# Kernel tuning notes

Hardware: AMD Instinct MI355X
Metric: run time of the kernel (lower is better)

The kernel has to match this reference:

```python
import jax, jax.numpy as jnp
import numpy as np

N = 50000   # nodes
E = 800000  # edges (before self-loops)
B = 256     # graphs in batch
F = 128     # input feature dim
H = 4       # heads per layer
C = 64      # out_channels per head
NEG_SLOPE = 0.2


def setup_inputs() -> dict:
    key = jax.random.key(0)
    ks = jax.random.split(key, 16)
    s = 0.05
    inp = {
        "x": jax.random.normal(ks[0], (N, F), dtype=jnp.float32),
        "edge_index": jax.random.randint(ks[1], (2, E), 0, N, dtype=jnp.int32),
        "batch": jnp.sort(jax.random.randint(ks[2], (N,), 0, B, dtype=jnp.int32)),
        # layer 1: F -> H*C
        "W1": jax.random.normal(ks[3], (F, H * C), dtype=jnp.float32) * s,
        "as1": jax.random.normal(ks[4], (H, C), dtype=jnp.float32) * s,
        "ad1": jax.random.normal(ks[5], (H, C), dtype=jnp.float32) * s,
        "b1": jnp.zeros((H * C,), dtype=jnp.float32),
        # layer 2: H*C -> H*C
        "W2": jax.random.normal(ks[6], (H * C, H * C), dtype=jnp.float32) * s,
        "as2": jax.random.normal(ks[7], (H, C), dtype=jnp.float32) * s,
        "ad2": jax.random.normal(ks[8], (H, C), dtype=jnp.float32) * s,
        "b2": jnp.zeros((H * C,), dtype=jnp.float32),
        # layer 3: H*C -> H*C
        "W3": jax.random.normal(ks[9], (H * C, H * C), dtype=jnp.float32) * s,
        "as3": jax.random.normal(ks[10], (H, C), dtype=jnp.float32) * s,
        "ad3": jax.random.normal(ks[11], (H, C), dtype=jnp.float32) * s,
        "b3": jnp.zeros((H * C,), dtype=jnp.float32),
    }
    return inp


def _gat_layer(x, src, dst, W, a_src, a_dst, bias):
    """PyG GATConv (concat=True, self-loops already included in src/dst)."""
    n = x.shape[0]
    xh = (x @ W).reshape(n, H, C)                      # [N,H,C]
    alpha_s = jnp.sum(xh * a_src, axis=-1)             # [N,H]
    alpha_d = jnp.sum(xh * a_dst, axis=-1)             # [N,H]
    logits = alpha_s[src] + alpha_d[dst]               # [E',H]
    logits = jnp.where(logits > 0, logits, NEG_SLOPE * logits)  # LeakyReLU
    # segment-wise softmax over destination neighborhoods
    m = jax.lax.stop_gradient(jax.ops.segment_max(logits, dst, num_segments=n))
    e = jnp.exp(logits - m[dst])
    z = jax.ops.segment_sum(e, dst, num_segments=n)
    alpha = e / (z[dst] + 1e-16)                       # [E',H]
    msg = xh[src] * alpha[:, :, None]                  # [E',H,C]
    out = jax.ops.segment_sum(msg, dst, num_segments=n)  # [N,H,C]
    return out.reshape(n, H * C) + bias


def reference(x, edge_index, batch, W1, as1, ad1, b1, W2, as2, ad2, b2, W3, as3, ad3, b3):
    n = x.shape[0]
    loops = jnp.arange(n, dtype=edge_index.dtype)
    src = jnp.concatenate([edge_index[0], loops])
    dst = jnp.concatenate([edge_index[1], loops])
    # dropout is identity at inference; activation = ReLU between layers
    h = jax.nn.relu(_gat_layer(x, src, dst, W1, as1, ad1, b1))
    h = jax.nn.relu(_gat_layer(h, src, dst, W2, as2, ad2, b2))
    h = _gat_layer(h, src, dst, W3, as3, ad3, b3)
    pooled = jax.ops.segment_max(h, batch, num_segments=B)  # global max pool -> [B, H*C]
    return jnp.squeeze(pooled)
```

## Files before the change

kernel.cpp:

```cpp
#include <hip/hip_runtime.h>
#include <hip/hip_fp16.h>
#include <math.h>

#define NN 50000
#define NE 800000
#define NT 850000
#define NB 256
#define FIN 128
#define HC 256
#define NH 4
#define CD 64
#define NEG 0.2f
#define SCAN_B 196
#define PSPL 8

typedef _Float16 half8 __attribute__((ext_vector_type(8)));
typedef _Float16 half4v __attribute__((ext_vector_type(4)));
typedef float f32x4 __attribute__((ext_vector_type(4)));

__device__ __forceinline__ void gld16(const void* g, void* l) {
    __builtin_amdgcn_global_load_lds(
        (const __attribute__((address_space(1))) void*)g,
        (__attribute__((address_space(3))) void*)l, 16, 0, 0);
}


__global__ void zero_int_kernel(int* __restrict__ p, int n) {
    int i = blockIdx.x * blockDim.x + threadIdx.x;
    if (i < n) p[i] = 0;
}

__global__ void hist_kernel(const int* __restrict__ ei, int* __restrict__ cnt) {
    int e = blockIdx.x * blockDim.x + threadIdx.x;
    if (e < NE) {
        atomicAdd(&cnt[ei[NE + e]], 1);
    } else if (e < NT) {
        atomicAdd(&cnt[e - NE], 1);
    }
}

__global__ __launch_bounds__(256) void part_kernel(const int* __restrict__ cnt,
                                                   int* __restrict__ part) {
    __shared__ int red[4];
    int i = blockIdx.x * 256 + threadIdx.x;
    int v = (i < NN) ? cnt[i] : 0;
#pragma unroll
    for (int off = 32; off > 0; off >>= 1) v += __shfl_down(v, off);
    if ((threadIdx.x & 63) == 0) red[threadIdx.x >> 6] = v;
    __syncthreads();
    if (threadIdx.x == 0) part[blockIdx.x] = red[0] + red[1] + red[2] + red[3];
}

__global__ __launch_bounds__(256) void offs_kernel(const int* __restrict__ part,
                                                   int* __restrict__ boff) {
    __shared__ int sh[256];
    int t = threadIdx.x;
    sh[t] = (t < SCAN_B) ? part[t] : 0;
    __syncthreads();
    for (int off = 1; off < 256; off <<= 1) {
        int add = (t >= off) ? sh[t - off] : 0;
        __syncthreads();
        sh[t] += add;
        __syncthreads();
    }
    boff[t] = (t == 0) ? 0 : sh[t - 1];
}

__global__ __launch_bounds__(256) void write_scan_kernel(const int* __restrict__ cnt,
        const int* __restrict__ boff, int* __restrict__ rowptr, int* __restrict__ cursor) {
    __shared__ int sh[256];
    int t = threadIdx.x;
    int i = blockIdx.x * 256 + t;
    int v = (i < NN) ? cnt[i] : 0;
    sh[t] = v;
    __syncthreads();
    for (int off = 1; off < 256; off <<= 1) {
        int add = (t >= off) ? sh[t - off] : 0;
        __syncthreads();
        sh[t] += add;
        __syncthreads();
    }
    int run = boff[blockIdx.x] + sh[t] - v;
    if (i < NN) { rowptr[i] = run; cursor[i] = run; }
    if (i == NN - 1) rowptr[NN] = run + v;
}

__global__ void scatter_kernel(const int* __restrict__ ei, int* __restrict__ cursor,
                               int* __restrict__ colsrc) {
    int e = blockIdx.x * blockDim.x + threadIdx.x;
    int s, d;
    if (e < NE)      { s = ei[e]; d = ei[NE + e]; }
    else if (e < NT) { s = e - NE; d = s; }
    else return;
    int pos = atomicAdd(&cursor[d], 1);
    colsrc[pos] = s;
}

__global__ void batch_bounds_kernel(const int* __restrict__ batch, int* __restrict__ bstart) {
    int i = blockIdx.x * blockDim.x + threadIdx.x;
    if (i >= NN) return;
    int b = batch[i];
    if (i == 0) {
        for (int bb = 0; bb <= b; ++bb) bstart[bb] = 0;
    } else {
        int pb = batch[i - 1];
        if (pb != b) for (int bb = pb + 1; bb <= b; ++bb) bstart[bb] = i;
    }
    if (i == NN - 1) {
        for (int bb = b + 1; bb <= NB; ++bb) bstart[bb] = NN;
    }
}


__global__ __launch_bounds__(256) void split_x_kernel(const float* __restrict__ X,
        _Float16* __restrict__ Xh, _Float16* __restrict__ Xl) {
    int i = blockIdx.x * 256 + threadIdx.x;
    if (i >= NN * FIN / 4) return;
    float4 v = reinterpret_cast<const float4*>(X)[i];
    half4v h, l;
    h[0] = (_Float16)v.x; h[1] = (_Float16)v.y; h[2] = (_Float16)v.z; h[3] = (_Float16)v.w;
    l[0] = (_Float16)(v.x - (float)h[0]);
    l[1] = (_Float16)(v.y - (float)h[1]);
    l[2] = (_Float16)(v.z - (float)h[2]);
    l[3] = (_Float16)(v.w - (float)h[3]);
    reinterpret_cast<half4v*>(Xh)[i] = h;
    reinterpret_cast<half4v*>(Xl)[i] = l;
}


template<int K>
__global__ __launch_bounds__(256) void wprep_kernel(const float* __restrict__ W,
                                                    _Float16* __restrict__ WtS) {
    __shared__ float sm[8][257];
    const int t = threadIdx.x;
    const int b = blockIdx.x;
    const int kb = b * 8;
    const bool lo3 = (kb >= 2 * K);
    const int kphys = lo3 ? kb - 2 * K : (kb >= K ? kb - K : kb);
#pragma unroll
    for (int i = 0; i < 8; ++i) {
        int idx = i * 256 + t;
        sm[idx >> 8][idx & 255] = W[(size_t)(kphys + (idx >> 8)) * HC + (idx & 255)];
    }
    __syncthreads();
    half8 o;
#pragma unroll
    for (int r = 0; r < 8; ++r) {
        float w = sm[r][t];
        _Float16 h = (_Float16)w;
        o[r] = lo3 ? (_Float16)(w - (float)h) : h;
    }
    *reinterpret_cast<half8*>(&WtS[((size_t)b * 256 + t) * 8]) = o;
}


template<int K>
__global__ __launch_bounds__(256) void mfma_gemm_kernel(
        const _Float16* __restrict__ Xh, const _Float16* __restrict__ Xl,
        const _Float16* __restrict__ WtS, __half* __restrict__ XHo,
        const float* __restrict__ as_g, const float* __restrict__ ad_g,
        float* __restrict__ aS, float* __restrict__ aD) {
    constexpr int C3 = 3 * K;
    constexpr int NSTEP = C3 / 32;
    constexpr int SPP = K / 32;
    __shared__ __align__(16) _Float16 As[4][64 * 32];
    __shared__ __align__(16) _Float16 Bs[4][32 * 256];
    const int t = threadIdx.x;
    const int lane = t & 63;
    const int wid = t >> 6;
    const int wm = wid & 1, wn = wid >> 1;
    const int r0 = blockIdx.x * 64;
    const int l15 = lane & 15;
    const int kcl = lane >> 4;
    const int kcA = t >> 6;
    const int arow = min(r0 + ((t & 63) ^ kcA), NN - 1);

    f32x4 acc[2][8];
#pragma unroll
    for (int i = 0; i < 2; ++i)
#pragma unroll
        for (int j = 0; j < 8; ++j) acc[i][j] = (f32x4)0.f;

    auto issue = [&](int s) {
        const int sel = s / SPP;
        const int cbase = (s - sel * SPP) * 32;
        const _Float16* srcA = (sel == 1) ? Xl : Xh;
        const int buf = s & 3;
        gld16(srcA + (size_t)arow * K + cbase + kcA * 8, &As[buf][t * 8]);
        const _Float16* bsrc = WtS + (size_t)s * (32 * 256);
#pragma unroll
        for (int r = 0; r < 4; ++r)
            gld16(bsrc + ((size_t)r * 256 + t) * 8, &Bs[buf][(r * 256 + t) * 8]);
    };
    auto mfma_step = [&](int s) {
        const int buf = s & 3;
        half8 a0 = *reinterpret_cast<const half8*>(
            &As[buf][(kcl * 64 + ((wm * 32      + l15) ^ kcl)) * 8]);
        half8 a1 = *reinterpret_cast<const half8*>(
            &As[buf][(kcl * 64 + ((wm * 32 + 16 + l15) ^ kcl)) * 8]);
        const _Float16* bp = &Bs[buf][(kcl * 256 + wn * 128 + l15) * 8];
        __builtin_amdgcn_s_setprio(1);
#pragma unroll
        for (int nf = 0; nf < 8; ++nf) {
            half8 b = *reinterpret_cast<const half8*>(bp + nf * 16 * 8);
            acc[0][nf] = __builtin_amdgcn_mfma_f32_16x16x32_f16(a0, b, acc[0][nf], 0, 0, 0);
            acc[1][nf] = __builtin_amdgcn_mfma_f32_16x16x32_f16(a1, b, acc[1][nf], 0, 0, 0);
        }
        __builtin_amdgcn_s_setprio(0);
    };

    issue(0); issue(1); issue(2);
    asm volatile("s_waitcnt vmcnt(10)" ::: "memory");
    __builtin_amdgcn_s_barrier();
    __builtin_amdgcn_sched_barrier(0);

    for (int s = 0; s < NSTEP - 3; ++s) {
        issue(s + 3);
        mfma_step(s);
        asm volatile("s_waitcnt vmcnt(10) lgkmcnt(0)" ::: "memory");
        __builtin_amdgcn_s_barrier();
        __builtin_amdgcn_sched_barrier(0);
    }
    mfma_step(NSTEP - 3);
    asm volatile("s_waitcnt vmcnt(5) lgkmcnt(0)" ::: "memory");
    __builtin_amdgcn_s_barrier();
    __builtin_amdgcn_sched_barrier(0);
    mfma_step(NSTEP - 2);
    asm volatile("s_waitcnt vmcnt(0) lgkmcnt(0)" ::: "memory");
    __builtin_amdgcn_s_barrier();
    __builtin_amdgcn_sched_barrier(0);
    mfma_step(NSTEP - 1);

    const int rb = r0 + wm * 32 + (lane >> 4) * 4;
    const int cb = wn * 128 + l15;
    float asv[8], adv[8];
#pragma unroll
    for (int nf = 0; nf < 8; ++nf) {
        asv[nf] = as_g[cb + nf * 16];
        adv[nf] = ad_g[cb + nf * 16];
    }
#pragma unroll
    for (int mf = 0; mf < 2; ++mf)
#pragma unroll
        for (int r = 0; r < 4; ++r) {
            int row = rb + mf * 16 + r;
            float s0 = 0.f, s1 = 0.f, d0 = 0.f, d1 = 0.f;
#pragma unroll
            for (int nf = 0; nf < 4; ++nf) {
                float a = acc[mf][nf][r], b = acc[mf][nf + 4][r];
                s0 += a * asv[nf];     d0 += a * adv[nf];
                s1 += b * asv[nf + 4]; d1 += b * adv[nf + 4];
            }
#pragma unroll
            for (int off = 1; off < 16; off <<= 1) {
                s0 += __shfl_xor(s0, off); s1 += __shfl_xor(s1, off);
                d0 += __shfl_xor(d0, off); d1 += __shfl_xor(d1, off);
            }
            if (row < NN) {
                if (l15 == 0) {
                    aS[row * 4 + 2 * wn] = s0; aS[row * 4 + 2 * wn + 1] = s1;
                    aD[row * 4 + 2 * wn] = d0; aD[row * 4 + 2 * wn + 1] = d1;
                }
#pragma unroll
                for (int nf = 0; nf < 8; ++nf)
                    XHo[(size_t)row * HC + cb + nf * 16] = __float2half(acc[mf][nf][r]);
            }
        }
}


#define LEAKY(v) ((v) > 0.f ? (v) : NEG * (v))

template<int RELU, int SPLIT>
__global__ __launch_bounds__(256) void aggregate_kernel(
        const int* __restrict__ rowptr, const int* __restrict__ colsrc,
        const float* __restrict__ aS, const float* __restrict__ aD,
        const __half* __restrict__ XH,
        const float* __restrict__ bias, float* __restrict__ OUT,
        __half* __restrict__ OUTh, __half* __restrict__ OUTl) {
    __shared__ float4 wbuf[4][64];
    __shared__ int    ibuf[4][64];
    const int wslot = threadIdx.x >> 6;
    int n = blockIdx.x * 4 + wslot;
    int lane = threadIdx.x & 63;
    bool lo = lane < 32;
    const __half2* xbase = reinterpret_cast<const __half2*>(XH);
    float4 adv = *reinterpret_cast<const float4*>(aD + n * 4);
    float zl = 0.f, zh = 0.f;
    float al0 = 0.f, al1 = 0.f, ah0 = 0.f, ah1 = 0.f;
    int jb = rowptr[n], je = rowptr[n + 1];
    for (int c0 = jb; c0 < je; c0 += 64) {
        int cnt = min(64, je - c0);
        {
            int e = min(c0 + lane, je - 1);
            int s = colsrc[e];
            float4 sv = *reinterpret_cast<const float4*>(aS + s * 4);
            float4 w;
            w.x = __expf(LEAKY(sv.x + adv.x));
            w.y = __expf(LEAKY(sv.y + adv.y));
            w.z = __expf(LEAKY(sv.z + adv.z));
            w.w = __expf(LEAKY(sv.w + adv.w));
            wbuf[wslot][lane] = w;
            ibuf[wslot][lane] = s;
        }
        int u = 0;
        for (; u + 8 <= cnt; u += 8) {
            int sidx[8];
            float4 w[8];
#pragma unroll
            for (int k = 0; k < 8; ++k) { sidx[k] = ibuf[wslot][u + k]; w[k] = wbuf[wslot][u + k]; }
            __half2 p[8], q[8];
#pragma unroll
            for (int k = 0; k < 8; ++k) {
                const __half2* xp = xbase + (size_t)sidx[k] * (HC / 2) + lane;
                p[k] = xp[0];
                q[k] = xp[64];
            }
#pragma unroll
            for (int k = 0; k < 8; ++k) {
                float wl = lo ? w[k].x : w[k].y, wh = lo ? w[k].z : w[k].w;
                float2 f = __half22float2(p[k]);
                al0 += wl * f.x; al1 += wl * f.y;
                f = __half22float2(q[k]);
                ah0 += wh * f.x; ah1 += wh * f.y;
                zl += wl; zh += wh;
            }
        }
        for (; u < cnt; ++u) {
            int s0 = ibuf[wslot][u];
            float4 w0 = wbuf[wslot][u];
            const __half2* xp = xbase + (size_t)s0 * (HC / 2) + lane;
            __half2 p0 = xp[0], q0 = xp[64];
            float w0l = lo ? w0.x : w0.y, w0h = lo ? w0.z : w0.w;
            float2 f = __half22float2(p0);
            al0 += w0l * f.x; al1 += w0l * f.y;
            f = __half22float2(q0);
            ah0 += w0h * f.x; ah1 += w0h * f.y;
            zl += w0l; zh += w0h;
        }
    }
    float izl = 1.f / (zl + 1e-16f), izh = 1.f / (zh + 1e-16f);
    float2 bl = reinterpret_cast<const float2*>(bias)[lane];
    float2 bh = reinterpret_cast<const float2*>(bias + 128)[lane];
    float o0 = al0 * izl + bl.x;
    float o1 = al1 * izl + bl.y;
    float o2 = ah0 * izh + bh.x;
    float o3 = ah1 * izh + bh.y;
    if (RELU) {
        o0 = fmaxf(o0, 0.f); o1 = fmaxf(o1, 0.f);
        o2 = fmaxf(o2, 0.f); o3 = fmaxf(o3, 0.f);
    }
    if (SPLIT) {
        __half h0 = __float2half(o0), h1 = __float2half(o1);
        __half h2 = __float2half(o2), h3 = __float2half(o3);
        __half2* ph = reinterpret_cast<__half2*>(OUTh + (size_t)n * HC) + lane;
        ph[0]  = __half2(h0, h1);
        ph[64] = __half2(h2, h3);
        __half2* pl = reinterpret_cast<__half2*>(OUTl + (size_t)n * HC) + lane;
        pl[0]  = __half2(__float2half(o0 - __half2float(h0)), __float2half(o1 - __half2float(h1)));
        pl[64] = __half2(__float2half(o2 - __half2float(h2)), __float2half(o3 - __half2float(h3)));
    } else {
        float2* op = reinterpret_cast<float2*>(OUT + (size_t)n * HC) + lane;
        op[0]  = make_float2(o0, o1);
        op[64] = make_float2(o2, o3);
    }
}


__global__ __launch_bounds__(256) void pool1_kernel(const float* __restrict__ Hf,
        const int* __restrict__ bstart, float* __restrict__ part) {
    int b = blockIdx.x / PSPL, sp = blockIdx.x % PSPL;
    int c = threadIdx.x;
    int i0 = bstart[b], i1 = bstart[b + 1];
    float m = -INFINITY;
    for (int i = i0 + sp; i < i1; i += PSPL) m = fmaxf(m, Hf[(size_t)i * HC + c]);
    part[(size_t)blockIdx.x * HC + c] = m;
}

__global__ __launch_bounds__(256) void pool2_kernel(const float* __restrict__ part,
        float* __restrict__ out) {
    int b = blockIdx.x;
    int c = threadIdx.x;
    float m = -INFINITY;
#pragma unroll
    for (int sp = 0; sp < PSPL; ++sp)
        m = fmaxf(m, part[(size_t)(b * PSPL + sp) * HC + c]);
    out[b * HC + c] = m;
}


extern "C" void kernel_launch(void* const* d_in, const int* in_sizes, int n_in,
                              void* d_out, int out_size, void* d_ws, size_t ws_size,
                              hipStream_t stream) {
    const float* x     = (const float*)d_in[0];
    const int*   ei    = (const int*)d_in[1];
    const int*   batch = (const int*)d_in[2];
    const float* W1  = (const float*)d_in[3];
    const float* as1 = (const float*)d_in[4];
    const float* ad1 = (const float*)d_in[5];
    const float* b1  = (const float*)d_in[6];
    const float* W2  = (const float*)d_in[7];
    const float* as2 = (const float*)d_in[8];
    const float* ad2 = (const float*)d_in[9];
    const float* b2  = (const float*)d_in[10];
    const float* W3  = (const float*)d_in[11];
    const float* as3 = (const float*)d_in[12];
    const float* ad3 = (const float*)d_in[13];
    const float* b3  = (const float*)d_in[14];
    float* out = (float*)d_out;

    __half* Hh  = (__half*)d_ws;
    __half* Hl  = Hh + (size_t)NN * HC;
    __half* XHh = Hl + (size_t)NN * HC;
    _Float16* Xh1 = (_Float16*)Hh;
    _Float16* Xl1 = Xh1 + (size_t)NN * FIN;
    float* bufB = (float*)Hh;
    _Float16* WtS = (_Float16*)(XHh + (size_t)NN * HC);
    float*  aS  = (float*)(WtS + 768 * 256);
    float*  aD  = aS + NN * NH;
    float*  ppart = aD + NN * NH;
    int* cnt    = (int*)(ppart + (size_t)NB * PSPL * HC);
    int* rowptr = cnt + NN;
    int* cursor = rowptr + (NN + 1);
    int* colsrc = cursor + NN;
    int* bstart = colsrc + NT;
    int* part   = bstart + (NB + 1);
    int* boff   = part + SCAN_B;

    zero_int_kernel<<<(NN + 255) / 256, 256, 0, stream>>>(cnt, NN);
    hist_kernel<<<(NT + 255) / 256, 256, 0, stream>>>(ei, cnt);
    part_kernel<<<SCAN_B, 256, 0, stream>>>(cnt, part);
    offs_kernel<<<1, 256, 0, stream>>>(part, boff);
    write_scan_kernel<<<SCAN_B, 256, 0, stream>>>(cnt, boff, rowptr, cursor);
    scatter_kernel<<<(NT + 255) / 256, 256, 0, stream>>>(ei, cursor, colsrc);
    batch_bounds_kernel<<<(NN + 255) / 256, 256, 0, stream>>>(batch, bstart);

    const int gemm_grid = (NN + 63) / 64;
    const int node_grid = NN / 4;

    split_x_kernel<<<(NN * FIN / 4 + 255) / 256, 256, 0, stream>>>(x, Xh1, Xl1);

    wprep_kernel<FIN><<<3 * FIN / 8, 256, 0, stream>>>(W1, WtS);
    mfma_gemm_kernel<FIN><<<gemm_grid, 256, 0, stream>>>(
        Xh1, Xl1, WtS, XHh, as1, ad1, aS, aD);
    aggregate_kernel<1, 1><<<node_grid, 256, 0, stream>>>(rowptr, colsrc, aS, aD, XHh, b1,
                                                          nullptr, Hh, Hl);

    wprep_kernel<HC><<<3 * HC / 8, 256, 0, stream>>>(W2, WtS);
    mfma_gemm_kernel<HC><<<gemm_grid, 256, 0, stream>>>(
        (_Float16*)Hh, (_Float16*)Hl, WtS, XHh, as2, ad2, aS, aD);
    aggregate_kernel<1, 1><<<node_grid, 256, 0, stream>>>(rowptr, colsrc, aS, aD, XHh, b2,
                                                          nullptr, Hh, Hl);

    wprep_kernel<HC><<<3 * HC / 8, 256, 0, stream>>>(W3, WtS);
    mfma_gemm_kernel<HC><<<gemm_grid, 256, 0, stream>>>(
        (_Float16*)Hh, (_Float16*)Hl, WtS, XHh, as3, ad3, aS, aD);
    aggregate_kernel<0, 0><<<node_grid, 256, 0, stream>>>(rowptr, colsrc, aS, aD, XHh, b3,
                                                          bufB, nullptr, nullptr);

    pool1_kernel<<<NB * PSPL, 256, 0, stream>>>(bufB, bstart, ppart);
    pool2_kernel<<<NB, 256, 0, stream>>>(ppart, out);
}
```

Measured before the change: 468.1 us.

## Fuse fp32 hi/lo split into GEMM A-load and restage pipeline through registers

Removes the separate split_x kernel and instead converts fp32 input to hi/lo fp16 inside the layer-1 GEMM while staging A through registers. The GEMM pipeline drops from four to three LDS buffers, and A tiles are written to LDS by threads rather than by direct global-to-LDS loads. This avoids a full round-trip of the split input through memory, at the cost of register pressure and a different latency-hiding structure. Each aggregation is also launched as two half-sized grids, which adds launch overhead.

```diff
diff --git a/kernel.cpp b/kernel.cpp
--- a/kernel.cpp
+++ b/kernel.cpp
@@ -15,7 +15,6 @@
 #define PSPL 8
 
 typedef _Float16 half8 __attribute__((ext_vector_type(8)));
-typedef _Float16 half4v __attribute__((ext_vector_type(4)));
 typedef float f32x4 __attribute__((ext_vector_type(4)));
 
 __device__ __forceinline__ void gld16(const void* g, void* l) {
@@ -112,22 +111,6 @@
 }
 
 
-__global__ __launch_bounds__(256) void split_x_kernel(const float* __restrict__ X,
-        _Float16* __restrict__ Xh, _Float16* __restrict__ Xl) {
-    int i = blockIdx.x * 256 + threadIdx.x;
-    if (i >= NN * FIN / 4) return;
-    float4 v = reinterpret_cast<const float4*>(X)[i];
-    half4v h, l;
-    h[0] = (_Float16)v.x; h[1] = (_Float16)v.y; h[2] = (_Float16)v.z; h[3] = (_Float16)v.w;
-    l[0] = (_Float16)(v.x - (float)h[0]);
-    l[1] = (_Float16)(v.y - (float)h[1]);
-    l[2] = (_Float16)(v.z - (float)h[2]);
-    l[3] = (_Float16)(v.w - (float)h[3]);
-    reinterpret_cast<half4v*>(Xh)[i] = h;
-    reinterpret_cast<half4v*>(Xl)[i] = l;
-}
-
-
 template<int K>
 __global__ __launch_bounds__(256) void wprep_kernel(const float* __restrict__ W,
                                                     _Float16* __restrict__ WtS) {
@@ -154,17 +137,18 @@
 }
 
 
-template<int K>
+template<int K, bool F32IN>
 __global__ __launch_bounds__(256) void mfma_gemm_kernel(
         const _Float16* __restrict__ Xh, const _Float16* __restrict__ Xl,
+        const float* __restrict__ Xf,
         const _Float16* __restrict__ WtS, __half* __restrict__ XHo,
         const float* __restrict__ as_g, const float* __restrict__ ad_g,
         float* __restrict__ aS, float* __restrict__ aD) {
     constexpr int C3 = 3 * K;
     constexpr int NSTEP = C3 / 32;
     constexpr int SPP = K / 32;
-    __shared__ __align__(16) _Float16 As[4][64 * 32];
-    __shared__ __align__(16) _Float16 Bs[4][32 * 256];
+    __shared__ __align__(16) _Float16 As[3][64 * 32];
+    __shared__ __align__(16) _Float16 Bs[3][32 * 256];
     const int t = threadIdx.x;
     const int lane = t & 63;
     const int wid = t >> 6;
@@ -172,8 +156,9 @@
     const int r0 = blockIdx.x * 64;
     const int l15 = lane & 15;
     const int kcl = lane >> 4;
-    const int kcA = t >> 6;
-    const int arow = min(r0 + ((t & 63) ^ kcA), NN - 1);
+    const int srowA = t >> 2;
+    const int skcA  = t & 3;
+    const int arow = min(r0 + srowA, NN - 1);
 
     f32x4 acc[2][8];
 #pragma unroll
@@ -181,19 +166,43 @@
 #pragma unroll
         for (int j = 0; j < 8; ++j) acc[i][j] = (f32x4)0.f;
 
-    auto issue = [&](int s) {
+    auto loadA = [&](int s, float4& v0, float4& v1) {
         const int sel = s / SPP;
         const int cbase = (s - sel * SPP) * 32;
-        const _Float16* srcA = (sel == 1) ? Xl : Xh;
-        const int buf = s & 3;
-        gld16(srcA + (size_t)arow * K + cbase + kcA * 8, &As[buf][t * 8]);
+        if constexpr (F32IN) {
+            const float* p = Xf + (size_t)arow * K + cbase + skcA * 8;
+            v0 = *reinterpret_cast<const float4*>(p);
+            v1 = *reinterpret_cast<const float4*>(p + 4);
+        } else {
+            const _Float16* src = (sel == 1) ? Xl : Xh;
+            v0 = *reinterpret_cast<const float4*>(src + (size_t)arow * K + cbase + skcA * 8);
+        }
+    };
+    auto writeA = [&](int s, int buf, float4 v0, float4 v1) {
+        _Float16* d = &As[buf][(skcA * 64 + (srowA ^ skcA)) * 8];
+        if constexpr (F32IN) {
+            const int sel = s / SPP;
+            float f[8];
+            *reinterpret_cast<float4*>(f) = v0;
+            *reinterpret_cast<float4*>(f + 4) = v1;
+            half8 h;
+#pragma unroll
+            for (int e = 0; e < 8; ++e) {
+                _Float16 a = (_Float16)f[e];
+                h[e] = (sel == 1) ? (_Float16)(f[e] - (float)a) : a;
+            }
+            *reinterpret_cast<half8*>(d) = h;
+        } else {
+            *reinterpret_cast<float4*>(d) = v0;
+        }
+    };
+    auto issueB = [&](int s, int buf) {
         const _Float16* bsrc = WtS + (size_t)s * (32 * 256);
 #pragma unroll
         for (int r = 0; r < 4; ++r)
             gld16(bsrc + ((size_t)r * 256 + t) * 8, &Bs[buf][(r * 256 + t) * 8]);
     };
-    auto mfma_step = [&](int s) {
-        const int buf = s & 3;
+    auto mfma_step = [&](int s, int buf) {
         half8 a0 = *reinterpret_cast<const half8*>(
             &As[buf][(kcl * 64 + ((wm * 32      + l15) ^ kcl)) * 8]);
         half8 a1 = *reinterpret_cast<const half8*>(
@@ -209,27 +218,34 @@
         __builtin_amdgcn_s_setprio(0);
     };
 
-    issue(0); issue(1); issue(2);
-    asm volatile("s_waitcnt vmcnt(10)" ::: "memory");
+    float4 a00, a01, aN1_0, aN1_1, aN2_0, aN2_1;
+    loadA(0, a00, a01);
+    issueB(0, 0);
+    loadA(1, aN1_0, aN1_1);
+    issueB(1, 1);
+    writeA(0, 0, a00, a01);
+    if constexpr (F32IN) asm volatile("s_waitcnt vmcnt(6) lgkmcnt(0)" ::: "memory");
+    else                 asm volatile("s_waitcnt vmcnt(5) lgkmcnt(0)" ::: "memory");
     __builtin_amdgcn_s_barrier();
     __builtin_amdgcn_sched_barrier(0);
 
-    for (int s = 0; s < NSTEP - 3; ++s) {
-        issue(s + 3);
-        mfma_step(s);
-        asm volatile("s_waitcnt vmcnt(10) lgkmcnt(0)" ::: "memory");
+    for (int s = 0; s < NSTEP - 2; ++s) {
+        loadA(s + 2, aN2_0, aN2_1);
+        issueB(s + 2, (s + 2) % 3);
+        mfma_step(s, s % 3);
+        writeA(s + 1, (s + 1) % 3, aN1_0, aN1_1);
+        if constexpr (F32IN) asm volatile("s_waitcnt vmcnt(6) lgkmcnt(0)" ::: "memory");
+        else                 asm volatile("s_waitcnt vmcnt(5) lgkmcnt(0)" ::: "memory");
         __builtin_amdgcn_s_barrier();
         __builtin_amdgcn_sched_barrier(0);
-    }
-    mfma_step(NSTEP - 3);
-    asm volatile("s_waitcnt vmcnt(5) lgkmcnt(0)" ::: "memory");
-    __builtin_amdgcn_s_barrier();
-    __builtin_amdgcn_sched_barrier(0);
-    mfma_step(NSTEP - 2);
+        aN1_0 = aN2_0; aN1_1 = aN2_1;
+    }
+    mfma_step(NSTEP - 2, (NSTEP - 2) % 3);
+    writeA(NSTEP - 1, (NSTEP - 1) % 3, aN1_0, aN1_1);
     asm volatile("s_waitcnt vmcnt(0) lgkmcnt(0)" ::: "memory");
     __builtin_amdgcn_s_barrier();
     __builtin_amdgcn_sched_barrier(0);
-    mfma_step(NSTEP - 1);
+    mfma_step(NSTEP - 1, (NSTEP - 1) % 3);
 
     const int rb = r0 + wm * 32 + (lane >> 4) * 4;
     const int cb = wn * 128 + l15;
@@ -273,6 +289,7 @@
 
 template<int RELU, int SPLIT>
 __global__ __launch_bounds__(256) void aggregate_kernel(
+        int nbase,
         const int* __restrict__ rowptr, const int* __restrict__ colsrc,
         const float* __restrict__ aS, const float* __restrict__ aD,
         const __half* __restrict__ XH,
@@ -281,7 +298,7 @@
     __shared__ float4 wbuf[4][64];
     __shared__ int    ibuf[4][64];
     const int wslot = threadIdx.x >> 6;
-    int n = blockIdx.x * 4 + wslot;
+    int n = nbase + blockIdx.x * 4 + wslot;
     int lane = threadIdx.x & 63;
     bool lo = lane < 32;
     const __half2* xbase = reinterpret_cast<const __half2*>(XH);
@@ -412,8 +429,6 @@
     __half* Hh  = (__half*)d_ws;
     __half* Hl  = Hh + (size_t)NN * HC;
     __half* XHh = Hl + (size_t)NN * HC;
-    _Float16* Xh1 = (_Float16*)Hh;
-    _Float16* Xl1 = Xh1 + (size_t)NN * FIN;
     float* bufB = (float*)Hh;
     _Float16* WtS = (_Float16*)(XHh + (size_t)NN * HC);
     float*  aS  = (float*)(WtS + 768 * 256);
@@ -436,26 +451,31 @@
     batch_bounds_kernel<<<(NN + 255) / 256, 256, 0, stream>>>(batch, bstart);
 
     const int gemm_grid = (NN + 63) / 64;
-    const int node_grid = NN / 4;
-
-    split_x_kernel<<<(NN * FIN / 4 + 255) / 256, 256, 0, stream>>>(x, Xh1, Xl1);
+    const int half_grid = NN / 8;
+    const int NHALF = NN / 2;
 
     wprep_kernel<FIN><<<3 * FIN / 8, 256, 0, stream>>>(W1, WtS);
-    mfma_gemm_kernel<FIN><<<gemm_grid, 256, 0, stream>>>(
-        Xh1, Xl1, WtS, XHh, as1, ad1, aS, aD);
-    aggregate_kernel<1, 1><<<node_grid, 256, 0, stream>>>(rowptr, colsrc, aS, aD, XHh, b1,
+    mfma_gemm_kernel<FIN, true><<<gemm_grid, 256, 0, stream>>>(
+        nullptr, nullptr, x, WtS, XHh, as1, ad1, aS, aD);
+    aggregate_kernel<1, 1><<<half_grid, 256, 0, stream>>>(0, rowptr, colsrc, aS, aD, XHh, b1,
                                                           nullptr, Hh, Hl);
+    aggregate_kernel<1, 1><<<half_grid, 256, 0, stream>>>(NHALF, rowptr, colsrc, aS, aD, XHh, b1,
+                                                          nullptr, Hh, Hl);
 
     wprep_kernel<HC><<<3 * HC / 8, 256, 0, stream>>>(W2, WtS);
-    mfma_gemm_kernel<HC><<<gemm_grid, 256, 0, stream>>>(
-        (_Float16*)Hh, (_Float16*)Hl, WtS, XHh, as2, ad2, aS, aD);
-    aggregate_kernel<1, 1><<<node_grid, 256, 0, stream>>>(rowptr, colsrc, aS, aD, XHh, b2,
+    mfma_gemm_kernel<HC, false><<<gemm_grid, 256, 0, stream>>>(
+        (_Float16*)Hh, (_Float16*)Hl, nullptr, WtS, XHh, as2, ad2, aS, aD);
+    aggregate_kernel<1, 1><<<half_grid, 256, 0, stream>>>(0, rowptr, colsrc, aS, aD, XHh, b2,
                                                           nullptr, Hh, Hl);
+    aggregate_kernel<1, 1><<<half_grid, 256, 0, stream>>>(NHALF, rowptr, colsrc, aS, aD, XHh, b2,
+                                                          nullptr, Hh, Hl);
 
     wprep_kernel<HC><<<3 * HC / 8, 256, 0, stream>>>(W3, WtS);
-    mfma_gemm_kernel<HC><<<gemm_grid, 256, 0, stream>>>(
-        (_Float16*)Hh, (_Float16*)Hl, WtS, XHh, as3, ad3, aS, aD);
-    aggregate_kernel<0, 0><<<node_grid, 256, 0, stream>>>(rowptr, colsrc, aS, aD, XHh, b3,
+    mfma_gemm_kernel<HC, false><<<gemm_grid, 256, 0, stream>>>(
+        (_Float16*)Hh, (_Float16*)Hl, nullptr, WtS, XHh, as3, ad3, aS, aD);
+    aggregate_kernel<0, 0><<<half_grid, 256, 0, stream>>>(0, rowptr, colsrc, aS, aD, XHh, b3,
+                                                          bufB, nullptr, nullptr);
+    aggregate_kernel<0, 0><<<half_grid, 256, 0, stream>>>(NHALF, rowptr, colsrc, aS, aD, XHh, b3,
                                                           bufB, nullptr, nullptr);
 
     pool1_kernel<<<NB * PSPL, 256, 0, stream>>>(bufB, bstart, ppart);
```

Result: slower. 489.4 us (+4.5%).
